# Performance work log

Hardware: AMD Instinct MI355X
Metric: run time of the kernel (lower is better)

The kernel has to match this reference:

```python
import jax, jax.numpy as jnp
import numpy as np

N, D_IN = 65536, 512
H1, H2, D_SH = 1024, 1024, 512   # shared net: num_nodes_shared = [1024, 1024, 512]
HI = 512                          # indiv hidden width, num_nodes_indiv = [512, 512]


def setup_inputs() -> dict:
    key = jax.random.key(0)
    ks = jax.random.split(key, 16)
    s = 0.02
    inp = {
        "input": jax.random.normal(ks[0], (N, D_IN), jnp.float32),
        "treatment": jax.random.randint(ks[1], (N,), 0, 2, jnp.int32),
        # shared net (hidden ReLU layers + linear output, all with bias)
        "W0": jax.random.normal(ks[2], (D_IN, H1), jnp.float32) * s,
        "b0": jnp.zeros((H1,), jnp.float32),
        "W1": jax.random.normal(ks[3], (H1, H2), jnp.float32) * s,
        "b1": jnp.zeros((H2,), jnp.float32),
        "W2": jax.random.normal(ks[4], (H2, D_SH), jnp.float32) * s,
        "b2": jnp.zeros((D_SH,), jnp.float32),
        # risk net 0 (output layer has no bias)
        "A0": jax.random.normal(ks[5], (D_SH, HI), jnp.float32) * s,
        "a0": jnp.zeros((HI,), jnp.float32),
        "A1": jax.random.normal(ks[6], (HI, HI), jnp.float32) * s,
        "a1": jnp.zeros((HI,), jnp.float32),
        "A2": jax.random.normal(ks[7], (HI, 1), jnp.float32) * s,
        # risk net 1
        "C0": jax.random.normal(ks[8], (D_SH, HI), jnp.float32) * s,
        "c0": jnp.zeros((HI,), jnp.float32),
        "C1": jax.random.normal(ks[9], (HI, HI), jnp.float32) * s,
        "c1": jnp.zeros((HI,), jnp.float32),
        "C2": jax.random.normal(ks[10], (HI, 1), jnp.float32) * s,
    }
    return inp


def _risk_net(h, U0, u0, U1, u1, U2):
    h = jax.nn.relu(h @ U0 + u0)
    h = jax.nn.relu(h @ U1 + u1)
    return h @ U2  # [N, 1], no output bias


def reference(input, treatment, W0, b0, W1, b1, W2, b2,
              A0, a0, A1, a1, A2, C0, c0, C1, c1, C2):
    # shared MLP
    h = jax.nn.relu(input @ W0 + b0)
    h = jax.nn.relu(h @ W1 + b1)
    out = h @ W2 + b2                     # [N, D_SH]
    # Binary expert routing. The torch code gathers samples per treatment,
    # runs each group through its own MLP and scatters results back; the
    # math is equivalent to applying both experts and selecting per sample.
    y0 = _risk_net(out, A0, a0, A1, a1, A2)[:, 0]  # [N]
    y1 = _risk_net(out, C0, c0, C1, c1, C2)[:, 0]  # [N]
    y = jnp.where(treatment == 0, y0, y1)          # [N]
    return (y, out)
```

## Files before the change

kernel.cpp:

```cpp
#include <hip/hip_runtime.h>
#include <hip/hip_bf16.h>
#include <stdint.h>

typedef short short8 __attribute__((ext_vector_type(8)));
typedef float f32x4 __attribute__((ext_vector_type(4)));

#define NSAMP 65536
#define AS1 __attribute__((address_space(1)))
#define AS3 __attribute__((address_space(3)))

__device__ __forceinline__ unsigned f2bf(float f) {
    union { float f; unsigned u; } v; v.f = f;
    unsigned u = v.u;
    u += 0x7fffu + ((u >> 16) & 1u);
    return u >> 16;
}

__device__ __forceinline__ void wr8(char* d, f32x4 a, f32x4 b) {
    short8 o;
    o[0] = (short)f2bf(a[0]); o[1] = (short)f2bf(a[1]);
    o[2] = (short)f2bf(a[2]); o[3] = (short)f2bf(a[3]);
    o[4] = (short)f2bf(b[0]); o[5] = (short)f2bf(b[1]);
    o[6] = (short)f2bf(b[2]); o[7] = (short)f2bf(b[3]);
    *(short8*)d = o;
}

struct PrepArgs {
    const float *W0, *W1, *W2, *A0, *C0, *A1, *C1, *a0v, *c0v;
    unsigned short *W0T, *W1T, *W2T, *RT0, *A1T, *C1T;
    float *bcat, *yout;
};
__device__ __forceinline__ void tr8(const float* __restrict__ W, unsigned short* __restrict__ WT,
                                    int N, int K, int n, int kb) {
    short8 o;
#pragma unroll
    for (int j = 0; j < 8; ++j) o[j] = (short)f2bf(W[(size_t)(kb * 8 + j) * N + n]);
    *(short8*)(WT + (size_t)n * K + kb * 8) = o;
}
__global__ void k_prep(PrepArgs p) {
    int i = blockIdx.x * blockDim.x + threadIdx.x;
    if (i < 65536)  { tr8(p.W0, p.W0T, 1024, 512,  i & 1023, i >> 10); return; }
    i -= 65536;
    if (i < 131072) { tr8(p.W1, p.W1T, 1024, 1024, i & 1023, i >> 10); return; }
    i -= 131072;
    if (i < 65536)  { tr8(p.W2, p.W2T, 512, 1024,  i & 511,  i >> 9);  return; }
    i -= 65536;
    if (i < 32768)  { tr8(p.A0, p.RT0, 512, 512,   i & 511,  i >> 9);  return; }
    i -= 32768;
    if (i < 32768)  { int n = i & 511; tr8(p.C0, p.RT0 + (size_t)512 * 512, 512, 512, n, i >> 9); return; }
    i -= 32768;
    if (i < 32768)  { tr8(p.A1, p.A1T, 512, 512,   i & 511,  i >> 9);  return; }
    i -= 32768;
    if (i < 32768)  { tr8(p.C1, p.C1T, 512, 512,   i & 511,  i >> 9);  return; }
    i -= 32768;
    if (i < 512)    { p.bcat[i] = p.a0v[i]; return; }
    i -= 512;
    if (i < 512)    { p.bcat[512 + i] = p.c0v[i]; return; }
    i -= 512;
    if (i < 65536)  { p.yout[i] = 0.f; return; }
}
#define PREP_TOTAL (65536 + 131072 + 65536 + 4 * 32768 + 512 + 512 + 65536)

template<int MODE>
__global__ __launch_bounds__(512, 2)
void k_gemm256(const void* __restrict__ Av, int lda,
               const unsigned short* __restrict__ BT, const unsigned short* __restrict__ BT2,
               const float* __restrict__ bias, const float* __restrict__ bias2,
               unsigned short* __restrict__ Cbf, float* __restrict__ Cf32,
               const float* __restrict__ w2, const float* __restrict__ w2b,
               const int* __restrict__ TRt, float* __restrict__ ydot,
               int Ncols, int K, int TPB)
{
    __shared__ __align__(16) char lds[131072];

    const int tid  = threadIdx.x;
    const int lane = tid & 63;
    const int wid  = tid >> 6;
    const int wr   = wid >> 2;
    const int wcn  = wid & 3;

    const int bid = (int)((blockIdx.x & 7) * 32 + (blockIdx.x >> 3));
    const int cls = bid % TPB;
    const int w   = bid / TPB;
    const int MSTEP = 256 / TPB;

    int n0e, cOff = 0, expert = 0;
    const unsigned short* Bsel = BT;
    if (MODE == 2) {
        expert = cls >> 1;
        n0e = (cls & 1) << 8;
        cOff = expert << 9;
        if (expert) Bsel = BT2;
    } else {
        n0e = cls << 8;
    }

    const int srow = tid >> 2;
    const int scs  = (tid & 3) ^ ((srow >> 1) & 3);
    const int ldst = wid * 1024;

    const unsigned short* gB0 = Bsel + (size_t)(n0e + srow) * K + scs * 8;
    const unsigned short* gB1 = gB0 + (size_t)128 * K;

    const unsigned short* Ab = (const unsigned short*)Av;
    const float*          Af = (const float*)Av;
    const size_t dA = (size_t)MSTEP * 256 * lda;
    const unsigned short* cA0 = Ab + (size_t)((w << 8) + srow) * lda + cOff + scs * 8;
    const unsigned short* cA1 = cA0 + (size_t)128 * lda;
    const float* cF = Af + (size_t)((w << 8) + srow) * lda + scs * 8;

#define STAGE_BLK(dbuf, blkoff, g0, g1, koff)                                            \
    do {                                                                                 \
        __builtin_amdgcn_global_load_lds((const AS1 void*)((g0) + (koff)),               \
                                         (AS3 void*)((dbuf) + (blkoff) + ldst), 16, 0, 0); \
        __builtin_amdgcn_global_load_lds((const AS1 void*)((g1) + (koff)),               \
                                         (AS3 void*)((dbuf) + (blkoff) + 8192 + ldst), 16, 0, 0); \
    } while (0)

    int aOff[8], bOff[4];
#pragma unroll
    for (int i = 0; i < 8; ++i) {
        int r = wr * 128 + i * 16 + (lane & 15);
        aOff[i] = r * 64 + ((((lane >> 4) ^ ((r >> 1) & 3))) << 4);
    }
#pragma unroll
    for (int j = 0; j < 4; ++j) {
        int r = wcn * 64 + j * 16 + (lane & 15);
        bOff[j] = r * 64 + ((((lane >> 4) ^ ((r >> 1) & 3))) << 4);
    }

    f32x4 acc[8][4];
#pragma unroll
    for (int i = 0; i < 8; ++i)
#pragma unroll
        for (int j = 0; j < 4; ++j) acc[i][j] = (f32x4)0.f;

    const int KT  = K >> 6;
    const int TOT = TPB * KT;

    f32x4 xr0, xr1, xr2, xr3;
    f32x4 yr0, yr1, yr2, yr3;

    if constexpr (MODE == 3) {
        xr0 = *(const f32x4*)(cF);                xr1 = *(const f32x4*)(cF + 4);
        xr2 = *(const f32x4*)(cF + 128 * lda);    xr3 = *(const f32x4*)(cF + 128 * lda + 4);
        STAGE_BLK(lds, 32768, gB0, gB1, 0);
        __builtin_amdgcn_sched_barrier(0);
        yr0 = *(const f32x4*)(cF + 32);             yr1 = *(const f32x4*)(cF + 36);
        yr2 = *(const f32x4*)(cF + 128 * lda + 32); yr3 = *(const f32x4*)(cF + 128 * lda + 36);
        STAGE_BLK(lds, 49152, gB0, gB1, 32);
        __builtin_amdgcn_sched_barrier(0);
        wr8(lds + tid * 16, xr0, xr1);
        wr8(lds + 8192 + tid * 16, xr2, xr3);
        asm volatile("s_waitcnt vmcnt(6)" ::: "memory");
        asm volatile("s_waitcnt lgkmcnt(0)" ::: "memory");
    } else {
        STAGE_BLK(lds, 0,     cA0, cA1, 0);
        STAGE_BLK(lds, 32768, gB0, gB1, 0);
        STAGE_BLK(lds, 16384, cA0, cA1, 32);
        STAGE_BLK(lds, 49152, gB0, gB1, 32);
        asm volatile("s_waitcnt vmcnt(4)" ::: "memory");
    }
    __builtin_amdgcn_s_barrier();
    __builtin_amdgcn_sched_barrier(0);

    short8 pa[4], pb[4];
#pragma unroll
    for (int i = 0; i < 4; ++i) pa[i] = *(const short8*)(lds + aOff[i]);
#pragma unroll
    for (int j = 0; j < 4; ++j) pb[j] = *(const short8*)(lds + 32768 + bOff[j]);

    int g = 0;
    for (int tau = 0; tau < TPB; ++tau) {
        const unsigned short* nA0 = cA0 + dA;
        const unsigned short* nA1 = cA1 + dA;
        const float* nF = cF + dA;

        for (int t = 0; t < KT; ++t, ++g) {
            char* sbuf = lds + (g & 1) * 65536;
            char* dbuf = lds + ((g + 1) & 1) * 65536;
            const bool inTile = (t + 1 < KT);
            const bool st = (g + 1 < TOT);
            const unsigned short* sA0 = inTile ? cA0 : nA0;
            const unsigned short* sA1 = inTile ? cA1 : nA1;
            const float* sF = inTile ? cF : nF;
            const int koff = inTile ? ((t + 1) << 6) : 0;
            short8 xa[4];

            if constexpr (MODE == 3) {
                wr8(sbuf + 16384 + tid * 16, yr0, yr1);
                wr8(sbuf + 16384 + 8192 + tid * 16, yr2, yr3);
                if (st) {
                    xr0 = *(const f32x4*)(sF + koff);               xr1 = *(const f32x4*)(sF + koff + 4);
                    xr2 = *(const f32x4*)(sF + 128 * lda + koff);   xr3 = *(const f32x4*)(sF + 128 * lda + koff + 4);
                    STAGE_BLK(dbuf, 32768, gB0, gB1, koff);
                    __builtin_amdgcn_sched_barrier(0);
                }
            } else {
                if (st) {
                    STAGE_BLK(dbuf, 0,     sA0, sA1, koff);
                    STAGE_BLK(dbuf, 32768, gB0, gB1, koff);
                }
            }
#pragma unroll
            for (int i = 0; i < 4; ++i) xa[i] = *(const short8*)(sbuf + aOff[4 + i]);
            __builtin_amdgcn_s_setprio(1);
#pragma unroll
            for (int i = 0; i < 4; ++i)
#pragma unroll
                for (int j = 0; j < 4; ++j)
                    acc[i][j] = __builtin_amdgcn_mfma_f32_16x16x32_bf16(pb[j], pa[i], acc[i][j], 0, 0, 0);
            __builtin_amdgcn_s_setprio(0);

            __builtin_amdgcn_s_setprio(1);
#pragma unroll
            for (int i = 0; i < 4; ++i)
#pragma unroll
                for (int j = 0; j < 4; ++j)
                    acc[4 + i][j] = __builtin_amdgcn_mfma_f32_16x16x32_bf16(pb[j], xa[i], acc[4 + i][j], 0, 0, 0);
            __builtin_amdgcn_s_setprio(0);
            if (st) {
                if constexpr (MODE == 3) { asm volatile("s_waitcnt vmcnt(6)" ::: "memory"); }
                else                     { asm volatile("s_waitcnt vmcnt(4)" ::: "memory"); }
            } else {
                asm volatile("s_waitcnt vmcnt(0)" ::: "memory");
            }
            if constexpr (MODE == 3) { asm volatile("s_waitcnt lgkmcnt(0)" ::: "memory"); }
            __builtin_amdgcn_sched_barrier(0);
            __builtin_amdgcn_s_barrier();
            __builtin_amdgcn_sched_barrier(0);

#pragma unroll
            for (int i = 0; i < 4; ++i) pa[i] = *(const short8*)(sbuf + 16384 + aOff[i]);
#pragma unroll
            for (int j = 0; j < 4; ++j) pb[j] = *(const short8*)(sbuf + 49152 + bOff[j]);
            if constexpr (MODE == 3) {
                if (st) {
                    yr0 = *(const f32x4*)(sF + koff + 32);             yr1 = *(const f32x4*)(sF + koff + 36);
                    yr2 = *(const f32x4*)(sF + 128 * lda + koff + 32); yr3 = *(const f32x4*)(sF + 128 * lda + koff + 36);
                    STAGE_BLK(dbuf, 49152, gB0, gB1, koff + 32);
                    __builtin_amdgcn_sched_barrier(0);
                }
            } else {
                if (st) {
                    STAGE_BLK(dbuf, 16384, sA0, sA1, koff + 32);
                    STAGE_BLK(dbuf, 49152, gB0, gB1, koff + 32);
                }
            }
            __builtin_amdgcn_s_setprio(1);
#pragma unroll
            for (int i = 0; i < 4; ++i)
#pragma unroll
                for (int j = 0; j < 4; ++j)
                    acc[i][j] = __builtin_amdgcn_mfma_f32_16x16x32_bf16(pb[j], pa[i], acc[i][j], 0, 0, 0);
            __builtin_amdgcn_s_setprio(0);

#pragma unroll
            for (int i = 0; i < 4; ++i) xa[i] = *(const short8*)(sbuf + 16384 + aOff[4 + i]);
            __builtin_amdgcn_s_setprio(1);
#pragma unroll
            for (int i = 0; i < 4; ++i)
#pragma unroll
                for (int j = 0; j < 4; ++j)
                    acc[4 + i][j] = __builtin_amdgcn_mfma_f32_16x16x32_bf16(pb[j], xa[i], acc[4 + i][j], 0, 0, 0);
            __builtin_amdgcn_s_setprio(0);
            if (st) {
                if constexpr (MODE == 3) {
                    asm volatile("s_waitcnt vmcnt(6)" ::: "memory");
                    wr8(dbuf + tid * 16, xr0, xr1);
                    wr8(dbuf + 8192 + tid * 16, xr2, xr3);
                    asm volatile("s_waitcnt lgkmcnt(0)" ::: "memory");
                } else {
                    asm volatile("s_waitcnt vmcnt(4)" ::: "memory");
                }
                __builtin_amdgcn_sched_barrier(0);
                __builtin_amdgcn_s_barrier();
                __builtin_amdgcn_sched_barrier(0);
#pragma unroll
                for (int i = 0; i < 4; ++i) pa[i] = *(const short8*)(dbuf + aOff[i]);
#pragma unroll
                for (int j = 0; j < 4; ++j) pb[j] = *(const short8*)(dbuf + 32768 + bOff[j]);
            }
        }

        const int m0 = (w + MSTEP * tau) << 8;
        if (MODE == 2) {
            const float* be = expert ? bias2 : bias;
            const float* we = expert ? w2b : w2;
            const int nb = n0e + wcn * 64 + ((lane >> 4) << 2);
            f32x4 bv[4], wv[4];
#pragma unroll
            for (int j = 0; j < 4; ++j) {
                bv[j] = *(const f32x4*)(be + nb + j * 16);
                wv[j] = *(const f32x4*)(we + nb + j * 16);
            }
#pragma unroll
            for (int i = 0; i < 8; ++i) {
                float p = 0.f;
#pragma unroll
                for (int j = 0; j < 4; ++j)
#pragma unroll
                    for (int r = 0; r < 4; ++r)
                        p += fmaxf(acc[i][j][r] + bv[j][r], 0.f) * wv[j][r];
                p += __shfl_xor(p, 16);
                p += __shfl_xor(p, 32);
                const int m = m0 + wr * 128 + i * 16 + (lane & 15);
                if (lane < 16 && TRt[m] == expert) atomicAdd(&ydot[m], p);
            }
        } else {
            const int nb = n0e + wcn * 64 + ((lane >> 4) << 2);
            f32x4 bv[4];
#pragma unroll
            for (int j = 0; j < 4; ++j) bv[j] = *(const f32x4*)(bias + nb + j * 16);
#pragma unroll
            for (int i = 0; i < 8; ++i) {
                const int m = m0 + wr * 128 + i * 16 + (lane & 15);
                unsigned short* pbc = Cbf + (size_t)m * Ncols + nb;
#pragma unroll
                for (int j = 0; j < 4; ++j) {
                    f32x4 v = acc[i][j] + bv[j];
                    if (MODE != 1) {
#pragma unroll
                        for (int r = 0; r < 4; ++r) v[r] = fmaxf(v[r], 0.f);
                    }
                    if (MODE == 1) *(f32x4*)(Cf32 + (size_t)m * Ncols + nb + j * 16) = v;
                    unsigned long long pk =
                        (unsigned long long)(f2bf(v[0]) | (f2bf(v[1]) << 16)) |
                        ((unsigned long long)(f2bf(v[2]) | (f2bf(v[3]) << 16)) << 32);
                    *(unsigned long long*)(pbc + j * 16) = pk;
                }
            }
        }

#pragma unroll
        for (int i = 0; i < 8; ++i)
#pragma unroll
            for (int j = 0; j < 4; ++j) acc[i][j] = (f32x4)0.f;
        cA0 = nA0; cA1 = nA1; cF = nF;
    }
#undef STAGE_BLK
}


extern "C" void kernel_launch(void* const* d_in, const int* in_sizes, int n_in,
                              void* d_out, int out_size, void* d_ws, size_t ws_size,
                              hipStream_t stream) {
    const float* X  = (const float*)d_in[0];
    const int*  TR  = (const int*)d_in[1];
    const float* W0 = (const float*)d_in[2];  const float* b0 = (const float*)d_in[3];
    const float* W1 = (const float*)d_in[4];  const float* b1 = (const float*)d_in[5];
    const float* W2 = (const float*)d_in[6];  const float* b2 = (const float*)d_in[7];
    const float* A0 = (const float*)d_in[8];  const float* a0 = (const float*)d_in[9];
    const float* A1 = (const float*)d_in[10]; const float* a1 = (const float*)d_in[11];
    const float* A2 = (const float*)d_in[12];
    const float* C0 = (const float*)d_in[13]; const float* c0 = (const float*)d_in[14];
    const float* C1 = (const float*)d_in[15]; const float* c1 = (const float*)d_in[16];
    const float* C2 = (const float*)d_in[17];

    float* y_out   = (float*)d_out;
    float* out_out = (float*)d_out + NSAMP;

    char* ws = (char*)d_ws;
    size_t off = 0;
    auto alloc = [&](size_t bytes) -> char* {
        char* p = ws + off;
        off += (bytes + 255) & ~(size_t)255;
        return p;
    };
    unsigned short* H1b = (unsigned short*)alloc((size_t)NSAMP * 1024 * 2);
    unsigned short* H2b = (unsigned short*)alloc((size_t)NSAMP * 1024 * 2);
    unsigned short* OUTb = H1b;
    unsigned short* R01  = H2b;
    unsigned short* W0T = (unsigned short*)alloc(512 * 1024 * 2);
    unsigned short* W1T = (unsigned short*)alloc(1024 * 1024 * 2);
    unsigned short* W2T = (unsigned short*)alloc(1024 * 512 * 2);
    unsigned short* RT0 = (unsigned short*)alloc(1024 * 512 * 2);
    unsigned short* A1T = (unsigned short*)alloc(512 * 512 * 2);
    unsigned short* C1T = (unsigned short*)alloc(512 * 512 * 2);
    float* bcat = (float*)alloc(1024 * 4);

    PrepArgs pa;
    pa.W0 = W0; pa.W1 = W1; pa.W2 = W2; pa.A0 = A0; pa.C0 = C0; pa.A1 = A1; pa.C1 = C1;
    pa.a0v = a0; pa.c0v = c0;
    pa.W0T = W0T; pa.W1T = W1T; pa.W2T = W2T; pa.RT0 = RT0; pa.A1T = A1T; pa.C1T = C1T;
    pa.bcat = bcat; pa.yout = y_out;
    k_prep<<<(PREP_TOTAL + 255) / 256, 256, 0, stream>>>(pa);

    k_gemm256<3><<<256, 512, 0, stream>>>((const void*)X, 512, W0T, nullptr, b0, nullptr,
                                          H1b, nullptr, nullptr, nullptr, nullptr, nullptr,
                                          1024, 512, 4);
    k_gemm256<0><<<256, 512, 0, stream>>>((const void*)H1b, 1024, W1T, nullptr, b1, nullptr,
                                          H2b, nullptr, nullptr, nullptr, nullptr, nullptr,
                                          1024, 1024, 4);
    k_gemm256<1><<<256, 512, 0, stream>>>((const void*)H2b, 1024, W2T, nullptr, b2, nullptr,
                                          OUTb, out_out, nullptr, nullptr, nullptr, nullptr,
                                          512, 1024, 2);

    k_gemm256<0><<<256, 512, 0, stream>>>((const void*)OUTb, 512, RT0, nullptr, bcat, nullptr,
                                          R01, nullptr, nullptr, nullptr, nullptr, nullptr,
                                          1024, 512, 4);

    k_gemm256<2><<<256, 512, 0, stream>>>((const void*)R01, 1024, A1T, C1T, a1, c1,
                                          nullptr, nullptr, A2, C2, TR, y_out,
                                          512, 512, 4);
}
```

Baseline: 555.4 us.

## Load A operand straight from global into registers for ReLU GEMMs

Adds a MODE 4 GEMM path in which each wave reads its A-fragment rows directly from global memory into registers, and only the weight (B) tiles are staged through LDS with a double buffer. The two hidden ReLU GEMMs (W1 and the combined risk first layer) now use this path. The aim is to halve LDS traffic and staging for the activation operand, so LDS bandwidth and capacity are freed for B. The cost is uncoalesced per-lane global loads for A with little latency hiding, since a full vmcnt(0) wait and a barrier come every k-step.

```diff
diff --git a/kernel.cpp b/kernel.cpp
--- a/kernel.cpp
+++ b/kernel.cpp
@@ -109,6 +109,9 @@
     const unsigned short* cA1 = cA0 + (size_t)128 * lda;
     const float* cF = Af + (size_t)((w << 8) + srow) * lda + scs * 8;
 
+    const unsigned short* gA4 = Ab + (size_t)((w << 8) + wr * 128 + (lane & 15)) * lda
+                                   + ((lane >> 4) << 3);
+
 #define STAGE_BLK(dbuf, blkoff, g0, g1, koff)                                            \
     do {                                                                                 \
         __builtin_amdgcn_global_load_lds((const AS1 void*)((g0) + (koff)),               \
@@ -137,6 +140,89 @@
 
     const int KT  = K >> 6;
     const int TOT = TPB * KT;
+
+    if constexpr (MODE == 4) {
+        STAGE_BLK(lds, 0,     gB0, gB1, 0);
+        STAGE_BLK(lds, 16384, gB0, gB1, 32);
+        asm volatile("s_waitcnt vmcnt(0)" ::: "memory");
+        __builtin_amdgcn_s_barrier();
+        __builtin_amdgcn_sched_barrier(0);
+
+        const unsigned short* wA = gA4;
+        int g = 0;
+        for (int tau = 0; tau < TPB; ++tau) {
+            for (int t = 0; t < KT; ++t, ++g) {
+                const char* sbuf = lds + (g & 1) * 32768;
+                char* dbuf = lds + ((g + 1) & 1) * 32768;
+                const bool st = (g + 1 < TOT);
+                const bool inTile = (t + 1 < KT);
+                const int koff0 = t << 6;
+                const int koffn = inTile ? ((t + 1) << 6) : 0;
+
+                short8 af0[8], af1[8];
+#pragma unroll
+                for (int i = 0; i < 8; ++i)
+                    af0[i] = *(const short8*)(wA + (size_t)i * 16 * lda + koff0);
+#pragma unroll
+                for (int i = 0; i < 8; ++i)
+                    af1[i] = *(const short8*)(wA + (size_t)i * 16 * lda + koff0 + 32);
+                if (st) {
+                    STAGE_BLK(dbuf, 0,     gB0, gB1, koffn);
+                    STAGE_BLK(dbuf, 16384, gB0, gB1, koffn + 32);
+                }
+                short8 bf[4];
+#pragma unroll
+                for (int j = 0; j < 4; ++j) bf[j] = *(const short8*)(sbuf + bOff[j]);
+                __builtin_amdgcn_s_setprio(1);
+#pragma unroll
+                for (int i = 0; i < 8; ++i)
+#pragma unroll
+                    for (int j = 0; j < 4; ++j)
+                        acc[i][j] = __builtin_amdgcn_mfma_f32_16x16x32_bf16(bf[j], af0[i], acc[i][j], 0, 0, 0);
+                __builtin_amdgcn_s_setprio(0);
+#pragma unroll
+                for (int j = 0; j < 4; ++j) bf[j] = *(const short8*)(sbuf + 16384 + bOff[j]);
+                __builtin_amdgcn_s_setprio(1);
+#pragma unroll
+                for (int i = 0; i < 8; ++i)
+#pragma unroll
+                    for (int j = 0; j < 4; ++j)
+                        acc[i][j] = __builtin_amdgcn_mfma_f32_16x16x32_bf16(bf[j], af1[i], acc[i][j], 0, 0, 0);
+                __builtin_amdgcn_s_setprio(0);
+                asm volatile("s_waitcnt vmcnt(0)" ::: "memory");
+                asm volatile("s_waitcnt lgkmcnt(0)" ::: "memory");
+                __builtin_amdgcn_sched_barrier(0);
+                __builtin_amdgcn_s_barrier();
+                __builtin_amdgcn_sched_barrier(0);
+            }
+            const int m0 = (w + MSTEP * tau) << 8;
+            const int nb = n0e + wcn * 64 + ((lane >> 4) << 2);
+            f32x4 bv[4];
+#pragma unroll
+            for (int j = 0; j < 4; ++j) bv[j] = *(const f32x4*)(bias + nb + j * 16);
+#pragma unroll
+            for (int i = 0; i < 8; ++i) {
+                const int m = m0 + wr * 128 + i * 16 + (lane & 15);
+                unsigned short* pbc = Cbf + (size_t)m * Ncols + nb;
+#pragma unroll
+                for (int j = 0; j < 4; ++j) {
+                    f32x4 v = acc[i][j] + bv[j];
+#pragma unroll
+                    for (int r = 0; r < 4; ++r) v[r] = fmaxf(v[r], 0.f);
+                    unsigned long long pk =
+                        (unsigned long long)(f2bf(v[0]) | (f2bf(v[1]) << 16)) |
+                        ((unsigned long long)(f2bf(v[2]) | (f2bf(v[3]) << 16)) << 32);
+                    *(unsigned long long*)(pbc + j * 16) = pk;
+                }
+            }
+#pragma unroll
+            for (int i = 0; i < 8; ++i)
+#pragma unroll
+                for (int j = 0; j < 4; ++j) acc[i][j] = (f32x4)0.f;
+            wA += dA;
+        }
+        return;
+    }
 
     f32x4 xr0, xr1, xr2, xr3;
     f32x4 yr0, yr1, yr2, yr3;
@@ -389,14 +475,14 @@
     k_gemm256<3><<<256, 512, 0, stream>>>((const void*)X, 512, W0T, nullptr, b0, nullptr,
                                           H1b, nullptr, nullptr, nullptr, nullptr, nullptr,
                                           1024, 512, 4);
-    k_gemm256<0><<<256, 512, 0, stream>>>((const void*)H1b, 1024, W1T, nullptr, b1, nullptr,
+    k_gemm256<4><<<256, 512, 0, stream>>>((const void*)H1b, 1024, W1T, nullptr, b1, nullptr,
                                           H2b, nullptr, nullptr, nullptr, nullptr, nullptr,
                                           1024, 1024, 4);
     k_gemm256<1><<<256, 512, 0, stream>>>((const void*)H2b, 1024, W2T, nullptr, b2, nullptr,
                                           OUTb, out_out, nullptr, nullptr, nullptr, nullptr,
                                           512, 1024, 2);
 
-    k_gemm256<0><<<256, 512, 0, stream>>>((const void*)OUTb, 512, RT0, nullptr, bcat, nullptr,
+    k_gemm256<4><<<256, 512, 0, stream>>>((const void*)OUTb, 512, RT0, nullptr, bcat, nullptr,
                                           R01, nullptr, nullptr, nullptr, nullptr, nullptr,
                                           1024, 512, 4);
 
```

New measurement: 831.3 us. +49.7%, slower.
